# Performance work log

Hardware: AMD Instinct MI355X
Metric: run time of the kernel (lower is better)

The kernel has to match this reference:

```python
import jax, jax.numpy as jnp
import numpy as np

NZ, NC = 100, 2
FEAT_NUMBER, FEATURE_DIM = 8192, 1024
B = 8192
BN_EPS = 1e-5
GUMBEL_EPS = 0.001
TEMP = 0.1


def _batchnorm(h, gamma, beta):
    # torch BatchNorm1d training mode: biased batch statistics
    mu = jnp.mean(h, axis=0, keepdims=True)
    var = jnp.var(h, axis=0, keepdims=True)
    return (h - mu) * jax.lax.rsqrt(var + BN_EPS) * gamma + beta


def setup_inputs() -> dict:
    key = jax.random.key(0)
    ks = jax.random.split(key, 16)
    def glorot(k, shape):
        lim = 1.0 / np.sqrt(shape[0])
        return jax.random.uniform(k, shape, jnp.float32, -lim, lim)
    return {
        "x": jax.random.normal(ks[0], (B, NZ), jnp.float32),
        "y": jax.random.uniform(ks[1], (B, NC), jnp.float32),
        "W1": glorot(ks[2], (NZ + NC, 256)), "b1": jnp.zeros((256,), jnp.float32),
        "g1": jnp.ones((256,), jnp.float32), "be1": jnp.zeros((256,), jnp.float32),
        "W2": glorot(ks[3], (256, 64)), "b2": jnp.zeros((64,), jnp.float32),
        "g2": jnp.ones((64,), jnp.float32), "be2": jnp.zeros((64,), jnp.float32),
        "W3": glorot(ks[4], (64, FEAT_NUMBER)), "b3": jnp.zeros((FEAT_NUMBER,), jnp.float32),
        "codebook": jax.random.normal(ks[5], (FEAT_NUMBER, FEATURE_DIM), jnp.float32),
    }


def reference(x, y, W1, b1, g1, be1, W2, b2, g2, be2, W3, b3, codebook):
    z = jnp.concatenate([x, y], axis=-1)                       # [B, nz+nc]
    h = jax.nn.relu(_batchnorm(z @ W1 + b1, g1, be1))          # [B, 256]
    h = jax.nn.relu(_batchnorm(h @ W2 + b2, g2, be2))          # [B, 64]
    logits = h @ W3 + b3                                       # [B, feat_number]

    # gumbel noise: U = eps*rand; g = -log(-log(U+eps)+eps)
    U = GUMBEL_EPS * jax.random.uniform(jax.random.key(42), logits.shape, jnp.float32)
    g = -jnp.log(-jnp.log(U + GUMBEL_EPS) + GUMBEL_EPS)
    y_soft = jax.nn.softmax((logits + g) / TEMP, axis=-1)

    # straight-through one-hot
    ind = jnp.argmax(y_soft, axis=-1)
    y_hard = jax.nn.one_hot(ind, FEAT_NUMBER, dtype=y_soft.dtype)
    z_st = jax.lax.stop_gradient(y_hard - y_soft) + y_soft     # [B, feat_number]

    # weighted codebook sum == matmul (avoids [B,F,D] broadcast intermediate)
    return jnp.einsum('bf,fd->bd', z_st, codebook)             # [B, feature_dim]
```

## Files before the change

### kernel.cpp

```cpp
#include <hip/hip_runtime.h>
#include <math.h>

#define B_ROWS   8192
#define NZ       100
#define NC       2
#define H1       256
#define H2       64
#define FEATN    8192
#define FDIM     1024
#define RROWS    16
#define NTILE    (FEATN / 16)
#define A1ROWS   16
#define A1BLKS   (B_ROWS / A1ROWS)
#define CONVBLKS 128
#define A2ROWS   16
#define A2BLKS   (B_ROWS / A2ROWS)

typedef __attribute__((ext_vector_type(8))) short short8;
typedef __attribute__((ext_vector_type(4))) float f32x4;

__device__ __forceinline__ unsigned rotl32(unsigned v, int r) {
    return (v << r) | (v >> (32 - r));
}
__device__ __forceinline__ unsigned threefry_bits(unsigned lo) {
    const unsigned ks0 = 0u, ks1 = 42u, ks2 = 0x1BD11BDAu ^ 42u;
    unsigned x0 = 0u + ks0;
    unsigned x1 = lo + ks1;
#define TF_R4(a,b,c,d) \
    x0 += x1; x1 = rotl32(x1,a); x1 ^= x0; \
    x0 += x1; x1 = rotl32(x1,b); x1 ^= x0; \
    x0 += x1; x1 = rotl32(x1,c); x1 ^= x0; \
    x0 += x1; x1 = rotl32(x1,d); x1 ^= x0;
    TF_R4(13,15,26,6);  x0 += ks1; x1 += ks2 + 1u;
    TF_R4(17,29,16,24); x0 += ks2; x1 += ks0 + 2u;
    TF_R4(13,15,26,6);  x0 += ks0; x1 += ks1 + 3u;
    TF_R4(17,29,16,24); x0 += ks1; x1 += ks2 + 4u;
    TF_R4(13,15,26,6);  x0 += ks2; x1 += ks0 + 5u;
#undef TF_R4
    return x0 ^ x1;
}
__device__ __forceinline__ float gumbel_g(unsigned flat) {
    unsigned bits = threefry_bits(flat);
    float u  = __uint_as_float((bits >> 9) | 0x3f800000u) - 1.0f;
    float U  = 0.001f * u;
    float t1 = U + 0.001f;
    float L1 = (float)log((double)t1);
    float A  = 0.001f - L1;
    float L2 = (float)log((double)A);
    return -L2;
}

__device__ __forceinline__ unsigned short f2bf(float x) {
    unsigned u = __float_as_uint(x);
    u += 0x7fffu + ((u >> 16) & 1u);
    return (unsigned short)(u >> 16);
}
__device__ __forceinline__ unsigned fmono(float x) {
    unsigned b = __float_as_uint(x);
    return (b & 0x80000000u) ? ~b : (b | 0x80000000u);
}

__global__ __launch_bounds__(512) void k_a1(
    const float* __restrict__ x, const float* __restrict__ y,
    const float* __restrict__ W1, const float* __restrict__ b1,
    const float* __restrict__ W3,
    float* __restrict__ a1, double* __restrict__ p1, double* __restrict__ p2,
    unsigned short* __restrict__ w3s, float* __restrict__ wmax)
{
    const int t = threadIdx.x;

    if (blockIdx.x >= A1BLKS) {
        const int job  = (blockIdx.x - A1BLKS) * 512 + t;
        const int T    = job >> 7;
        const int rem  = job & 127;
        const int kh   = rem >> 6;
        const int l    = rem & 63;
        const int quad = l >> 4, col = l & 15;
        const float* src = W3 + (size_t)(kh * 32 + quad * 8) * FEATN + T * 16 + col;
        unsigned short v[8];
        float mx = 0.0f;
#pragma unroll
        for (int jj = 0; jj < 8; ++jj) {
            float xv = src[(size_t)jj * FEATN];
            mx = fmaxf(mx, fabsf(xv));
            v[jj] = f2bf(xv);
        }
        uint4 o;
        o.x = (unsigned)v[0] | ((unsigned)v[1] << 16);
        o.y = (unsigned)v[2] | ((unsigned)v[3] << 16);
        o.z = (unsigned)v[4] | ((unsigned)v[5] << 16);
        o.w = (unsigned)v[6] | ((unsigned)v[7] << 16);
        ((uint4*)w3s)[job] = o;
#pragma unroll
        for (int off = 32; off; off >>= 1) mx = fmaxf(mx, __shfl_xor(mx, off));
        __shared__ float wred[8];
        if ((t & 63) == 0) wred[t >> 6] = mx;
        __syncthreads();
        if (t == 0) {
            float m = wred[0];
#pragma unroll
            for (int wq = 1; wq < 8; ++wq) m = fmaxf(m, wred[wq]);
            wmax[blockIdx.x - A1BLKS] = m;
        }
        return;
    }

    const int j    = t & 255;
    const int half = t >> 8;
    const int b0   = blockIdx.x * A1ROWS;
    const int r0   = half * 8;

    __shared__ __align__(16) float xs[NZ][16];
    __shared__ __align__(16) float ys[NC][16];
    __shared__ float vsh[256][8];
    for (int q = t; q < A1ROWS * NZ; q += 512) {
        int r = q / NZ, i = q - r * NZ;
        xs[i][r] = x[(size_t)b0 * NZ + q];
    }
    if (t < A1ROWS * NC) {
        int r = t >> 1, i = t & 1;
        ys[i][r] = y[b0 * NC + t];
    }
    __syncthreads();

    float acc[8];
#pragma unroll
    for (int r = 0; r < 8; ++r) acc[r] = 0.0f;
    for (int i = 0; i < NZ; ++i) {
        float wd = W1[i * H1 + j];
        const float4 x0 = *(const float4*)&xs[i][r0];
        const float4 x1 = *(const float4*)&xs[i][r0 + 4];
        acc[0] = fmaf(x0.x, wd, acc[0]); acc[1] = fmaf(x0.y, wd, acc[1]);
        acc[2] = fmaf(x0.z, wd, acc[2]); acc[3] = fmaf(x0.w, wd, acc[3]);
        acc[4] = fmaf(x1.x, wd, acc[4]); acc[5] = fmaf(x1.y, wd, acc[5]);
        acc[6] = fmaf(x1.z, wd, acc[6]); acc[7] = fmaf(x1.w, wd, acc[7]);
    }
#pragma unroll
    for (int i = 0; i < NC; ++i) {
        float wd = W1[(NZ + i) * H1 + j];
        const float4 y0 = *(const float4*)&ys[i][r0];
        const float4 y1 = *(const float4*)&ys[i][r0 + 4];
        acc[0] = fmaf(y0.x, wd, acc[0]); acc[1] = fmaf(y0.y, wd, acc[1]);
        acc[2] = fmaf(y0.z, wd, acc[2]); acc[3] = fmaf(y0.w, wd, acc[3]);
        acc[4] = fmaf(y1.x, wd, acc[4]); acc[5] = fmaf(y1.y, wd, acc[5]);
        acc[6] = fmaf(y1.z, wd, acc[6]); acc[7] = fmaf(y1.w, wd, acc[7]);
    }
    const float bb = b1[j];
    float v[8];
#pragma unroll
    for (int r = 0; r < 8; ++r) {
        v[r] = acc[r] + bb;
        a1[(b0 + r0 + r) * H1 + j] = v[r];
    }
    if (half) {
#pragma unroll
        for (int r = 0; r < 8; ++r) vsh[j][r] = v[r];
    }
    __syncthreads();
    if (!half) {
        double s = 0.0, s2 = 0.0;
#pragma unroll
        for (int r = 0; r < 8; ++r) {
            double dv = (double)v[r];
            s += dv; s2 += dv * dv;
        }
#pragma unroll
        for (int r = 0; r < 8; ++r) {
            double dv = (double)vsh[j][r];
            s += dv; s2 += dv * dv;
        }
        p1[blockIdx.x * H1 + j] = s;
        p2[blockIdx.x * H1 + j] = s2;
    }
}

__global__ __launch_bounds__(512) void k_stats(
    const double* __restrict__ p1, const double* __restrict__ p2,
    int nprt, int ncol,
    const float* __restrict__ gamma, const float* __restrict__ beta,
    float* __restrict__ scale, float* __restrict__ shift)
{
    const int t  = threadIdx.x;
    const int c  = t & 15, pg = t >> 4;
    const int j  = blockIdx.x * 16 + c;
    double s = 0.0, s2 = 0.0;
    for (int part = pg; part < nprt; part += 32) {
        s  += p1[(size_t)part * ncol + j];
        s2 += p2[(size_t)part * ncol + j];
    }
    __shared__ double ls[32][16], ls2[32][16];
    ls[pg][c] = s; ls2[pg][c] = s2;
    __syncthreads();
#pragma unroll
    for (int h = 16; h >= 1; h >>= 1) {
        if (pg < h) {
            ls[pg][c]  += ls[pg + h][c];
            ls2[pg][c] += ls2[pg + h][c];
        }
        __syncthreads();
    }
    if (t < 16) {
        const int jj = blockIdx.x * 16 + t;
        double S  = ls[0][t];
        double S2 = ls2[0][t];
        double mean = S * (1.0 / B_ROWS);
        double var  = S2 * (1.0 / B_ROWS) - mean * mean;
        double rstd = 1.0 / sqrt(var + 1e-5);
        double sc   = (double)gamma[jj] * rstd;
        scale[jj] = (float)sc;
        shift[jj] = (float)((double)beta[jj] - mean * sc);
    }
}

__global__ __launch_bounds__(512) void k_a2(
    const float* __restrict__ a1,
    const float* __restrict__ sc1, const float* __restrict__ sh1,
    const float* __restrict__ W2, const float* __restrict__ b2,
    float* __restrict__ a2, double* __restrict__ p1, double* __restrict__ p2)
{
    const int t  = threadIdx.x;
    const int k  = t & 63;
    const int rg = t >> 6;
    const int b0 = blockIdx.x * A2ROWS;
    const int r0 = rg * 2;

    __shared__ __align__(8) float hs[H1][18];
    __shared__ float vsh[64][17];

    {
        const int jc = t & 255, rq = t >> 8;
        const float sct = sc1[jc], sht = sh1[jc];
#pragma unroll
        for (int rr = rq * 8; rr < rq * 8 + 8; ++rr) {
            float vv = a1[(size_t)(b0 + rr) * H1 + jc];
            hs[jc][rr] = fmaxf(fmaf(vv, sct, sht), 0.0f);
        }
    }
    __syncthreads();

    float acc0 = 0.0f, acc1 = 0.0f;
#pragma unroll 4
    for (int j = 0; j < H1; ++j) {
        float wd = W2[j * H2 + k];
        const float2 h2 = *(const float2*)&hs[j][r0];
        acc0 = fmaf(h2.x, wd, acc0);
        acc1 = fmaf(h2.y, wd, acc1);
    }
    const float bb = b2[k];
    float v0 = acc0 + bb;
    float v1 = acc1 + bb;
    a2[(b0 + r0 + 0) * H2 + k] = v0;
    a2[(b0 + r0 + 1) * H2 + k] = v1;
    vsh[k][r0]     = v0;
    vsh[k][r0 + 1] = v1;
    __syncthreads();
    if (t < 64) {
        double s = 0.0, s2 = 0.0;
#pragma unroll
        for (int r = 0; r < A2ROWS; ++r) {
            double dv = (double)vsh[t][r];
            s += dv; s2 += dv * dv;
        }
        p1[blockIdx.x * H2 + t] = s;
        p2[blockIdx.x * H2 + t] = s2;
    }
}

__global__ __launch_bounds__(512)
__attribute__((amdgpu_waves_per_eu(4, 4)))
void k_main(
    const float* __restrict__ a2,
    const float* __restrict__ sc2, const float* __restrict__ sh2,
    const float* __restrict__ W3, const float* __restrict__ b3,
    const unsigned short* __restrict__ w3s, const float* __restrict__ wmax,
    const float* __restrict__ codebook, float* __restrict__ out)
{
    const int t    = threadIdx.x;
    const int wv   = t >> 6;
    const int lane = t & 63;
    const int quad = lane >> 4, col = lane & 15;
    const int b0   = blockIdx.x * RROWS;

    __shared__ __align__(16) float h2T[64][17];
    __shared__ float fineT[NTILE][17];
    __shared__ float thrS[RROWS];
    __shared__ unsigned long long best[RROWS];
    __shared__ unsigned short wl[RROWS * NTILE];
    __shared__ int wlN;
    __shared__ int rowInd[RROWS];
    __shared__ float maxwS;
    __shared__ float mparts[2];

    if (t == 0) wlN = 0;
    if (t < 128) {
        float m = wmax[t];
#pragma unroll
        for (int off = 32; off; off >>= 1) m = fmaxf(m, __shfl_xor(m, off));
        if ((t & 63) == 0) mparts[t >> 6] = m;
    }
    for (int q = t; q < RROWS * 64; q += 512) {
        int j = q >> 4, r = q & 15;
        float v = a2[(b0 + r) * H2 + j];
        h2T[j][r] = fmaxf(fmaf(v, sc2[j], sh2[j]), 0.0f);
    }
    __syncthreads();
    if (t == 0) maxwS = fmaxf(mparts[0], mparts[1]);

    short8 aF0, aF1;
#pragma unroll
    for (int jj = 0; jj < 8; ++jj) {
        aF0[jj] = (short)f2bf(h2T[quad * 8 + jj][col]);
        aF1[jj] = (short)f2bf(h2T[32 + quad * 8 + jj][col]);
    }

    {
        const uint4*  wp = (const uint4*)w3s + (size_t)wv * 8192 + lane;
        const float4* bq = (const float4*)b3 + wv * 256 + quad;
        for (int s = 0; s < 8; ++s) {
#pragma unroll
            for (int hu = 0; hu < 2; ++hu) {
                uint4 c[4], d[4];
                float4 bb[4];
#pragma unroll
                for (int u = 0; u < 4; ++u) {
                    const int uu = hu * 4 + u;
                    c[u]  = wp[uu * 128];
                    d[u]  = wp[uu * 128 + 64];
                    bb[u] = bq[uu * 4];
                }
#pragma unroll
                for (int u = 0; u < 4; ++u) {
                    f32x4 acc = {bb[u].x, bb[u].y, bb[u].z, bb[u].w};
                    acc = __builtin_amdgcn_mfma_f32_16x16x32_bf16(
                              *(const short8*)&c[u], aF0, acc, 0, 0, 0);
                    acc = __builtin_amdgcn_mfma_f32_16x16x32_bf16(
                              *(const short8*)&d[u], aF1, acc, 0, 0, 0);
                    float m = fmaxf(fmaxf(acc[0], acc[1]), fmaxf(acc[2], acc[3]));
                    m = fmaxf(m, __shfl_xor(m, 16));
                    m = fmaxf(m, __shfl_xor(m, 32));
                    if (lane < 16)
                        fineT[(wv * 8 + s) * 8 + hu * 4 + u][lane] = m;
                }
            }
            wp += 1024; bq += 32;
        }
    }
    __syncthreads();

    {
        const int r = t >> 5, cc = t & 31;
        float s = fabsf(h2T[2 * cc][r]) + fabsf(h2T[2 * cc + 1][r]);
        float gmv = -1e30f;
#pragma unroll
        for (int k = 0; k < 16; ++k) gmv = fmaxf(gmv, fineT[cc + 32 * k][r]);
#pragma unroll
        for (int off = 1; off < 32; off <<= 1) {
            s   += __shfl_xor(s, off);
            gmv  = fmaxf(gmv, __shfl_xor(gmv, off));
        }
        if (cc == 0) {
            float e = s * maxwS * (1.0f / 256.0f);
            thrS[r] = gmv - (0.1068f + e + 1e-3f);
            best[r] = 0ull;
        }
    }
    __syncthreads();

    {
        const int r = t >> 5, cc = t & 31;
        const float th = thrS[r];
#pragma unroll
        for (int k = 0; k < 16; ++k) {
            const int T = cc + 32 * k;
            if (fineT[T][r] >= th) {
                int idx = atomicAdd(&wlN, 1);
                wl[idx] = (unsigned short)((r << 9) | T);
            }
        }
    }
    __syncthreads();

    {
        const int n = wlN;
        const int g = lane >> 4;
        for (int i = wv * 4; i < n; i += 32) {
            const int  ci  = i + g;
            const bool act = (ci < n);
            const int  e   = act ? wl[ci] : 0;
            const int  r   = e >> 9;
            const int  T   = e & 511;
            const int  f   = T * 16 + col;
            float acc = b3[f];
            const float* wcol = W3 + f;
#pragma unroll 8
            for (int j = 0; j < 64; ++j) {
                acc = fmaf(h2T[j][r], *wcol, acc);
                wcol += FEATN;
            }
            if (act && acc >= thrS[r]) {
                float sc = acc + gumbel_g((unsigned)(b0 + r) * (unsigned)FEATN + (unsigned)f);
                unsigned long long pk = ((unsigned long long)fmono(sc) << 32)
                                      | (unsigned)(FEATN - 1 - f);
                atomicMax(&best[r], pk);
            }
        }
    }
    __syncthreads();
    if (t < RROWS) {
        rowInd[t] = (FEATN - 1 - (int)(best[t] & 0xFFFFFFFFull)) & (FEATN - 1);
    }
    __syncthreads();

    {
        const int rr = t >> 8, tt = t & 255;
        for (int rp = 0; rp < RROWS / 2; ++rp) {
            const int r = rp * 2 + rr;
            const int ind = rowInd[r];
            const float4* src = (const float4*)(codebook + (size_t)ind * FDIM);
            float4*       dst = (float4*)(out + (size_t)(b0 + r) * FDIM);
            dst[tt] = src[tt];
        }
    }
}

extern "C" void kernel_launch(void* const* d_in, const int* in_sizes, int n_in,
                              void* d_out, int out_size, void* d_ws, size_t ws_size,
                              hipStream_t stream)
{
    const float* x   = (const float*)d_in[0];
    const float* y   = (const float*)d_in[1];
    const float* W1  = (const float*)d_in[2];
    const float* b1  = (const float*)d_in[3];
    const float* g1  = (const float*)d_in[4];
    const float* be1 = (const float*)d_in[5];
    const float* W2  = (const float*)d_in[6];
    const float* b2  = (const float*)d_in[7];
    const float* g2  = (const float*)d_in[8];
    const float* be2 = (const float*)d_in[9];
    const float* W3  = (const float*)d_in[10];
    const float* b3  = (const float*)d_in[11];
    const float* cb  = (const float*)d_in[12];
    float* out = (float*)d_out;

    float* ws  = (float*)d_ws;
    float* a1  = ws;
    float* a2  = a1 + B_ROWS * H1;
    float* sc1 = a2 + B_ROWS * H2;
    float* sh1 = sc1 + H1;
    float* sc2 = sh1 + H1;
    float* sh2 = sc2 + H2;
    double* p1 = (double*)(sh2 + H2);
    double* p2 = p1 + A1BLKS * H1;
    unsigned short* w3s = (unsigned short*)(p2 + A1BLKS * H1);
    float* wmax = (float*)(w3s + NTILE * 2 * 64 * 8);

    k_a1   <<<A1BLKS + CONVBLKS, 512, 0, stream>>>(x, y, W1, b1, W3,
                                                   a1, p1, p2, w3s, wmax);
    k_stats<<<H1 / 16, 512, 0, stream>>>(p1, p2, A1BLKS, H1, g1, be1, sc1, sh1);
    k_a2   <<<A2BLKS, 512, 0, stream>>>(a1, sc1, sh1, W2, b2, a2, p1, p2);
    k_stats<<<H2 / 16, 512, 0, stream>>>(p1, p2, A2BLKS, H2, g2, be2, sc2, sh2);
    k_main <<<B_ROWS / RROWS, 512, 0, stream>>>(a2, sc2, sh2, W3, b3,
                                                w3s, wmax, cb, out);
}
```

Before: 207.5 us.

## Replace BN stats kernels with atomic partial sums and fold finalization into consumers

Drops the two separate k_stats reduction kernels. Producer blocks now atomically add their per-column sum and sum-of-squares (double) into 8 slotted accumulators, cleared by a memset. Each consumer block re-derives scale and shift from those 8 slots into shared memory. This removes two kernel launches and the partial-sum round trip. In exchange it adds a memset, double-precision atomics, and a small amount of redundant stats work in every consumer block, and the summation order is no longer deterministic.

```diff
diff --git a/kernel.cpp b/kernel.cpp
--- a/kernel.cpp
+++ b/kernel.cpp
@@ -64,7 +64,7 @@
     const float* __restrict__ x, const float* __restrict__ y,
     const float* __restrict__ W1, const float* __restrict__ b1,
     const float* __restrict__ W3,
-    float* __restrict__ a1, double* __restrict__ p1, double* __restrict__ p2,
+    float* __restrict__ a1, double* __restrict__ S1, double* __restrict__ S2,
     unsigned short* __restrict__ w3s, float* __restrict__ wmax)
 {
     const int t = threadIdx.x;
@@ -169,54 +169,18 @@
             double dv = (double)vsh[j][r];
             s += dv; s2 += dv * dv;
         }
-        p1[blockIdx.x * H1 + j] = s;
-        p2[blockIdx.x * H1 + j] = s2;
-    }
-}
-
-__global__ __launch_bounds__(512) void k_stats(
-    const double* __restrict__ p1, const double* __restrict__ p2,
-    int nprt, int ncol,
-    const float* __restrict__ gamma, const float* __restrict__ beta,
-    float* __restrict__ scale, float* __restrict__ shift)
-{
-    const int t  = threadIdx.x;
-    const int c  = t & 15, pg = t >> 4;
-    const int j  = blockIdx.x * 16 + c;
-    double s = 0.0, s2 = 0.0;
-    for (int part = pg; part < nprt; part += 32) {
-        s  += p1[(size_t)part * ncol + j];
-        s2 += p2[(size_t)part * ncol + j];
-    }
-    __shared__ double ls[32][16], ls2[32][16];
-    ls[pg][c] = s; ls2[pg][c] = s2;
-    __syncthreads();
-#pragma unroll
-    for (int h = 16; h >= 1; h >>= 1) {
-        if (pg < h) {
-            ls[pg][c]  += ls[pg + h][c];
-            ls2[pg][c] += ls2[pg + h][c];
-        }
-        __syncthreads();
-    }
-    if (t < 16) {
-        const int jj = blockIdx.x * 16 + t;
-        double S  = ls[0][t];
-        double S2 = ls2[0][t];
-        double mean = S * (1.0 / B_ROWS);
-        double var  = S2 * (1.0 / B_ROWS) - mean * mean;
-        double rstd = 1.0 / sqrt(var + 1e-5);
-        double sc   = (double)gamma[jj] * rstd;
-        scale[jj] = (float)sc;
-        shift[jj] = (float)((double)beta[jj] - mean * sc);
+        const int slot = blockIdx.x & 7;
+        atomicAdd(&S1[slot * H1 + j], s);
+        atomicAdd(&S2[slot * H1 + j], s2);
     }
 }
 
 __global__ __launch_bounds__(512) void k_a2(
     const float* __restrict__ a1,
-    const float* __restrict__ sc1, const float* __restrict__ sh1,
+    const float* __restrict__ g1, const float* __restrict__ be1,
+    const double* __restrict__ S1, const double* __restrict__ S2,
     const float* __restrict__ W2, const float* __restrict__ b2,
-    float* __restrict__ a2, double* __restrict__ p1, double* __restrict__ p2)
+    float* __restrict__ a2, double* __restrict__ S1b, double* __restrict__ S2b)
 {
     const int t  = threadIdx.x;
     const int k  = t & 63;
@@ -226,10 +190,27 @@
 
     __shared__ __align__(8) float hs[H1][18];
     __shared__ float vsh[64][17];
+    __shared__ float scs[H1], shs[H1];
+
+    if (t < H1) {
+        double s = 0.0, s2 = 0.0;
+#pragma unroll
+        for (int p = 0; p < 8; ++p) {
+            s  += S1[p * H1 + t];
+            s2 += S2[p * H1 + t];
+        }
+        double mean = s * (1.0 / B_ROWS);
+        double var  = s2 * (1.0 / B_ROWS) - mean * mean;
+        double rstd = 1.0 / sqrt(var + 1e-5);
+        double sc   = (double)g1[t] * rstd;
+        scs[t] = (float)sc;
+        shs[t] = (float)((double)be1[t] - mean * sc);
+    }
+    __syncthreads();
 
     {
         const int jc = t & 255, rq = t >> 8;
-        const float sct = sc1[jc], sht = sh1[jc];
+        const float sct = scs[jc], sht = shs[jc];
 #pragma unroll
         for (int rr = rq * 8; rr < rq * 8 + 8; ++rr) {
             float vv = a1[(size_t)(b0 + rr) * H1 + jc];
@@ -261,8 +242,9 @@
             double dv = (double)vsh[t][r];
             s += dv; s2 += dv * dv;
         }
-        p1[blockIdx.x * H2 + t] = s;
-        p2[blockIdx.x * H2 + t] = s2;
+        const int slot = blockIdx.x & 7;
+        atomicAdd(&S1b[slot * H2 + t], s);
+        atomicAdd(&S2b[slot * H2 + t], s2);
     }
 }
 
@@ -270,7 +252,8 @@
 __attribute__((amdgpu_waves_per_eu(4, 4)))
 void k_main(
     const float* __restrict__ a2,
-    const float* __restrict__ sc2, const float* __restrict__ sh2,
+    const float* __restrict__ g2, const float* __restrict__ be2,
+    const double* __restrict__ S1b, const double* __restrict__ S2b,
     const float* __restrict__ W3, const float* __restrict__ b3,
     const unsigned short* __restrict__ w3s, const float* __restrict__ wmax,
     const float* __restrict__ codebook, float* __restrict__ out)
@@ -290,6 +273,7 @@
     __shared__ int rowInd[RROWS];
     __shared__ float maxwS;
     __shared__ float mparts[2];
+    __shared__ float sc2S[H2], sh2S[H2];
 
     if (t == 0) wlN = 0;
     if (t < 128) {
@@ -298,10 +282,25 @@
         for (int off = 32; off; off >>= 1) m = fmaxf(m, __shfl_xor(m, off));
         if ((t & 63) == 0) mparts[t >> 6] = m;
     }
+    if (t < H2) {
+        double s = 0.0, s2 = 0.0;
+#pragma unroll
+        for (int p = 0; p < 8; ++p) {
+            s  += S1b[p * H2 + t];
+            s2 += S2b[p * H2 + t];
+        }
+        double mean = s * (1.0 / B_ROWS);
+        double var  = s2 * (1.0 / B_ROWS) - mean * mean;
+        double rstd = 1.0 / sqrt(var + 1e-5);
+        double sc   = (double)g2[t] * rstd;
+        sc2S[t] = (float)sc;
+        sh2S[t] = (float)((double)be2[t] - mean * sc);
+    }
+    __syncthreads();
     for (int q = t; q < RROWS * 64; q += 512) {
         int j = q >> 4, r = q & 15;
         float v = a2[(b0 + r) * H2 + j];
-        h2T[j][r] = fmaxf(fmaf(v, sc2[j], sh2[j]), 0.0f);
+        h2T[j][r] = fmaxf(fmaf(v, sc2S[j], sh2S[j]), 0.0f);
     }
     __syncthreads();
     if (t == 0) maxwS = fmaxf(mparts[0], mparts[1]);
@@ -445,20 +444,18 @@
     float* ws  = (float*)d_ws;
     float* a1  = ws;
     float* a2  = a1 + B_ROWS * H1;
-    float* sc1 = a2 + B_ROWS * H2;
-    float* sh1 = sc1 + H1;
-    float* sc2 = sh1 + H1;
-    float* sh2 = sc2 + H2;
-    double* p1 = (double*)(sh2 + H2);
-    double* p2 = p1 + A1BLKS * H1;
-    unsigned short* w3s = (unsigned short*)(p2 + A1BLKS * H1);
-    float* wmax = (float*)(w3s + NTILE * 2 * 64 * 8);
-
-    k_a1   <<<A1BLKS + CONVBLKS, 512, 0, stream>>>(x, y, W1, b1, W3,
-                                                   a1, p1, p2, w3s, wmax);
-    k_stats<<<H1 / 16, 512, 0, stream>>>(p1, p2, A1BLKS, H1, g1, be1, sc1, sh1);
-    k_a2   <<<A2BLKS, 512, 0, stream>>>(a1, sc1, sh1, W2, b2, a2, p1, p2);
-    k_stats<<<H2 / 16, 512, 0, stream>>>(p1, p2, A2BLKS, H2, g2, be2, sc2, sh2);
-    k_main <<<B_ROWS / RROWS, 512, 0, stream>>>(a2, sc2, sh2, W3, b3,
-                                                w3s, wmax, cb, out);
-}
+    double* S1  = (double*)(a2 + B_ROWS * H2);
+    double* S2  = S1 + 8 * H1;
+    double* S1b = S2 + 8 * H1;
+    double* S2b = S1b + 8 * H2;
+    unsigned short* w3s = (unsigned short*)(S2b + 8 * H2);
+    float* wmax = (float*)(w3s + H2 * FEATN);
+
+    hipMemsetAsync(S1, 0, (8 * H1 * 2 + 8 * H2 * 2) * sizeof(double), stream);
+    k_a1 <<<A1BLKS + CONVBLKS, 512, 0, stream>>>(x, y, W1, b1, W3,
+                                                 a1, S1, S2, w3s, wmax);
+    k_a2 <<<A2BLKS, 512, 0, stream>>>(a1, g1, be1, S1, S2, W2, b2,
+                                      a2, S1b, S2b);
+    k_main <<<B_ROWS / RROWS, 512, 0, stream>>>(a2, g2, be2, S1b, S2b,
+                                                W3, b3, w3s, wmax, cb, out);
+}
```

Result: faster. 199.7 us (-3.8%).
